# Performance work log

Measured on AMD Instinct MI355X. Metric: run time of the kernel, lower is better.

Reference implementation:

```python
import jax, jax.numpy as jnp
import numpy as np

VOCAB, E, H, P, B, S = 30522, 1024, 1024, 16, 32, 256
HD = H // 2  # per-direction LSTM hidden


def _lstm_dir(xt, Wih, Whh, bih, bhh, reverse):
    # xt: [S,B,in]; PyTorch gate order i,f,g,o
    Hd = Whh.shape[1]
    Bz = xt.shape[1]
    bias = bih + bhh

    def step(carry, xb):
        h, c = carry
        g = xb @ Wih.T + h @ Whh.T + bias
        i, f, gg, o = jnp.split(g, 4, axis=-1)
        c = jax.nn.sigmoid(f) * c + jax.nn.sigmoid(i) * jnp.tanh(gg)
        h = jax.nn.sigmoid(o) * jnp.tanh(c)
        return (h, c), h

    init = (jnp.zeros((Bz, Hd), xt.dtype), jnp.zeros((Bz, Hd), xt.dtype))
    _, hs = jax.lax.scan(step, init, xt, reverse=reverse)
    return hs  # [S,B,Hd], time-ordered


def _bilstm(x, Wih, Whh, bih, bhh):
    # x: [B,S,in]; Wih: [2,4*HD,in] (dir 0 = fwd, dir 1 = bwd)
    xt = jnp.swapaxes(x, 0, 1)
    fw = _lstm_dir(xt, Wih[0], Whh[0], bih[0], bhh[0], False)
    bw = _lstm_dir(xt, Wih[1], Whh[1], bih[1], bhh[1], True)
    return jnp.swapaxes(jnp.concatenate([fw, bw], axis=-1), 0, 1)  # [B,S,2*HD]


def setup_inputs() -> dict:
    key = jax.random.key(0)
    ks = jax.random.split(key, 20)
    sc = 0.05
    inp = {}
    inp["emb"] = jax.random.normal(ks[0], (VOCAB, E), jnp.float32) * sc
    inp["ctx_emb"] = jax.random.normal(ks[1], (VOCAB, E), jnp.float32) * sc
    inp["prompt_emb"] = jax.random.normal(ks[2], (P, E), jnp.float32) * sc
    # LSTM layer 0: input E; layer 1: input 2*HD = H
    inp["Wih0"] = jax.random.normal(ks[3], (2, 4 * HD, E), jnp.float32) * sc
    inp["Whh0"] = jax.random.normal(ks[4], (2, 4 * HD, HD), jnp.float32) * sc
    inp["bih0"] = jax.random.normal(ks[5], (2, 4 * HD), jnp.float32) * sc
    inp["bhh0"] = jax.random.normal(ks[6], (2, 4 * HD), jnp.float32) * sc
    inp["Wih1"] = jax.random.normal(ks[7], (2, 4 * HD, H), jnp.float32) * sc
    inp["Whh1"] = jax.random.normal(ks[8], (2, 4 * HD, HD), jnp.float32) * sc
    inp["bih1"] = jax.random.normal(ks[9], (2, 4 * HD), jnp.float32) * sc
    inp["bhh1"] = jax.random.normal(ks[10], (2, 4 * HD), jnp.float32) * sc
    inp["W1"] = jax.random.normal(ks[11], (H, H), jnp.float32) * sc
    inp["b1"] = jnp.zeros((H,), jnp.float32)
    inp["W2"] = jax.random.normal(ks[12], (E, H), jnp.float32) * sc
    inp["b2"] = jnp.zeros((E,), jnp.float32)
    inp["input_ids"] = jax.random.randint(ks[13], (B, S), 0, VOCAB)
    # distinct, sorted prompt positions per batch row (torch loop assumes valid slots)
    pk = jax.random.split(ks[14], B)
    perms = jax.vmap(lambda k: jax.random.permutation(k, S)[:P])(pk)
    inp["prompt_indexes"] = jnp.sort(perms, axis=1)
    return inp


def reference(emb, ctx_emb, prompt_emb, Wih0, Whh0, bih0, bhh0,
              Wih1, Whh1, bih1, bhh1, W1, b1, W2, b2,
              input_ids, prompt_indexes):
    raw = emb[input_ids]                               # [B,S,E]
    b_idx = jnp.arange(input_ids.shape[0])[:, None]    # [B,1]
    # unique_prompt branch: detached raw + ctx embedding, scatter prompt embeds
    allb = jax.lax.stop_gradient(raw) + ctx_emb[input_ids]
    allb = allb.at[b_idx, prompt_indexes].set(
        jnp.broadcast_to(prompt_emb, (input_ids.shape[0],) + prompt_emb.shape))
    h = _bilstm(allb, Wih0, Whh0, bih0, bhh0)
    h = _bilstm(h, Wih1, Whh1, bih1, bhh1)             # [B,S,H]
    out = jax.nn.relu(h @ W1.T + b1) @ W2.T + b2       # [B,S,E]
    upd = out[b_idx, prompt_indexes] + prompt_emb      # [B,P,E]
    return raw.at[b_idx, prompt_indexes].set(upd)
```

## Files before the change

kernel.cpp:

```cpp
#include <hip/hip_runtime.h>
#include <hip/hip_bf16.h>
#include <math.h>

constexpr int NB  = 32;
constexpr int NS  = 256;
constexpr int NE  = 1024;
constexpr int NH  = 1024;
constexpr int NHD = 512;
constexpr int NG  = 2048;
constexpr int NP  = 16;
constexpr int NBS = NB * NS;
constexpr int GK  = 1024;

constexpr int UPW  = 16;
constexpr int NWGD = NHD / UPW;
constexpr size_t GT_DIR = (size_t)NWGD * 256 * 2048;

typedef __attribute__((ext_vector_type(8))) short bf16x8;
typedef __attribute__((ext_vector_type(4))) float f32x4;
typedef unsigned short u16;

__device__ __forceinline__ float sigm(float x) { return 1.0f / (1.0f + __expf(-x)); }
__device__ __forceinline__ u16 f2bf(float f) {
    union { float f; unsigned u; } v; v.f = f;
    unsigned r = v.u + 0x7FFF + ((v.u >> 16) & 1);
    return (u16)(r >> 16);
}
__device__ __forceinline__ float bf2f(u16 b) {
    return __uint_as_float((unsigned)b << 16);
}

__global__ void k_zero(int* p) { p[blockIdx.x * 256 + threadIdx.x] = 0; }

__global__ void k_allb(const float* __restrict__ emb, const float* __restrict__ ctx,
                       const float* __restrict__ pemb, const int* __restrict__ ids,
                       const int* __restrict__ pidx, u16* __restrict__ allb) {
    int r = blockIdx.x;
    int b = r >> 8, s = r & 255;
    __shared__ int ppos;
    if (threadIdx.x == 0) {
        int t = -1;
        #pragma unroll
        for (int p = 0; p < NP; ++p)
            if (pidx[b * NP + p] == s) t = p;
        ppos = t;
    }
    __syncthreads();
    int e = threadIdx.x;
    float4 v;
    if (ppos >= 0) {
        v = ((const float4*)(pemb + (size_t)ppos * NE))[e];
    } else {
        int id = ids[r];
        float4 a = ((const float4*)(emb + (size_t)id * NE))[e];
        float4 c = ((const float4*)(ctx + (size_t)id * NE))[e];
        v = make_float4(a.x + c.x, a.y + c.y, a.z + c.z, a.w + c.w);
    }
    ushort4 o;
    o.x = f2bf(v.x); o.y = f2bf(v.y); o.z = f2bf(v.z); o.w = f2bf(v.w);
    *(ushort4*)(allb + ((size_t)(s * NB + b)) * NE + e * 4) = o;
}

__global__ void k_raw(const float* __restrict__ emb, const int* __restrict__ ids,
                      float* __restrict__ out) {
    int r = blockIdx.x;
    int id = ids[r];
    ((float4*)(out + (size_t)r * NE))[threadIdx.x] =
        ((const float4*)(emb + (size_t)id * NE))[threadIdx.x];
}

__global__ void k_wcvt(const float* __restrict__ Wih, const float* __restrict__ bih,
                       const float* __restrict__ bhh, u16* __restrict__ Wbf,
                       float* __restrict__ biasC) {
    int blk = blockIdx.x;
    int d = blk >> 11, np = blk & 2047;
    int rw = (np & 3) * 512 + (np >> 2);
    const float* src = Wih + ((size_t)d * NG + rw) * GK;
    u16* dst = Wbf + ((size_t)d * NG + np) * GK;
    int t = threadIdx.x;
    float4 v = ((const float4*)src)[t];
    ushort4 o;
    o.x = f2bf(v.x); o.y = f2bf(v.y); o.z = f2bf(v.z); o.w = f2bf(v.w);
    ((ushort4*)dst)[t] = o;
    if (t == 0)
        biasC[d * NG + np] = bih[d * NG + rw] + bhh[d * NG + rw];
}

__global__ __launch_bounds__(256) void k_gemm_m(const u16* __restrict__ A0,
                                                const u16* __restrict__ A1,
                                                int astride,
                                                const u16* __restrict__ W,
                                                const float* __restrict__ bc,
                                                float* __restrict__ Gt) {
    __shared__ char At[128 * 128];
    __shared__ char Wt[128 * 128];
    int tid = threadIdx.x;
    int lane = tid & 63, w = tid >> 6;
    int n0 = blockIdx.x * 128, m0 = blockIdx.y * 128;
    int r = tid >> 1, h = tid & 1;

    f32x4 acc[4][4];
    #pragma unroll
    for (int i = 0; i < 4; ++i)
        #pragma unroll
        for (int j = 0; j < 4; ++j) acc[i][j] = (f32x4){0.f, 0.f, 0.f, 0.f};

    unsigned rsw = (unsigned)((r & 7) << 4);
    for (int kt = 0; kt < GK; kt += 64) {
        {
            int k0 = kt + h * 32;
            const u16* asrc = (k0 < 512) ? (A0 + (size_t)(m0 + r) * astride + k0)
                                         : (A1 + (size_t)(m0 + r) * astride + (k0 - 512));
            const u16* wsrc = W + (size_t)(n0 + r) * GK + k0;
            #pragma unroll
            for (int j = 0; j < 4; ++j) {
                uint4 va = *(const uint4*)(asrc + j * 8);
                *(uint4*)(At + r * 128 + (((unsigned)(h * 64 + j * 16)) ^ rsw)) = va;
                uint4 vw = *(const uint4*)(wsrc + j * 8);
                *(uint4*)(Wt + r * 128 + (((unsigned)(h * 64 + j * 16)) ^ rsw)) = vw;
            }
        }
        __syncthreads();
        #pragma unroll
        for (int sub = 0; sub < 2; ++sub) {
            bf16x8 af[4], bfr[4];
            int kbyte = sub * 64 + (lane >> 4) * 16;
            #pragma unroll
            for (int ni = 0; ni < 4; ++ni) {
                int rr = (w & 1) * 64 + ni * 16 + (lane & 15);
                af[ni] = *(const bf16x8*)(Wt + rr * 128 + ((unsigned)kbyte ^ ((unsigned)((rr & 7) << 4))));
            }
            #pragma unroll
            for (int mi = 0; mi < 4; ++mi) {
                int rr = (w >> 1) * 64 + mi * 16 + (lane & 15);
                bfr[mi] = *(const bf16x8*)(At + rr * 128 + ((unsigned)kbyte ^ ((unsigned)((rr & 7) << 4))));
            }
            #pragma unroll
            for (int mi = 0; mi < 4; ++mi)
                #pragma unroll
                for (int ni = 0; ni < 4; ++ni)
                    acc[mi][ni] = __builtin_amdgcn_mfma_f32_16x16x32_bf16(
                        af[ni], bfr[mi], acc[mi][ni], 0, 0, 0);
        }
        __syncthreads();
    }
    #pragma unroll
    for (int mi = 0; mi < 4; ++mi) {
        int mp = m0 + (w >> 1) * 64 + mi * 16 + (lane & 15);
        int t = mp >> 5, b = mp & 31;
        #pragma unroll
        for (int ni = 0; ni < 4; ++ni) {
            int npb = n0 + (w & 1) * 64 + ni * 16 + (lane >> 4) * 4;
            int unit = npb >> 2;
            float4 bv = *(const float4*)(bc + npb);
            f32x4 a = acc[mi][ni];
            float4 o = make_float4(a[0] + bv.x, a[1] + bv.y, a[2] + bv.z, a[3] + bv.w);
            *(float4*)(Gt + ((size_t)((unit >> 4) * NS + t)) * 2048 + b * 64 + (unit & 15) * 4) = o;
        }
    }
}

__global__ __launch_bounds__(256) void k_lstm_p(const float* __restrict__ Gt,
                                                const float* __restrict__ Whh,
                                                u16* __restrict__ hxb,
                                                int* __restrict__ cblk) {
    __shared__ char hlds[NB * NHD * 2];
    int wg = blockIdx.x;
    int d = wg & 1;
    int slice = wg >> 1;
    int n0 = slice * UPW;
    int tid = threadIdx.x;
    int lane = tid & 63;
    int w = tid >> 6;
    int* lines  = cblk + d * 512;
    int* myline = lines + slice * 16;
    int pollidx = (lane & 31) * 16;
    u16* hxd = hxb + (size_t)d * NS * NB * NHD;
    const float* Gd = Gt + (size_t)d * GT_DIR + (size_t)slice * NS * 2048;

    bf16x8 wfrag[16];
    {
        int rloc = lane & 15;
        int usub = rloc >> 2, g = rloc & 3;
        int kb = lane >> 4;
        const float* wrow = Whh + ((size_t)d * NG + g * NHD + n0 + 4 * w + usub) * NHD;
        #pragma unroll
        for (int kk = 0; kk < 16; ++kk) {
            const float* p = wrow + kk * 32 + kb * 8;
            float4 x = *(const float4*)p;
            float4 y = *(const float4*)(p + 4);
            bf16x8 wf;
            wf[0] = (short)f2bf(x.x); wf[1] = (short)f2bf(x.y);
            wf[2] = (short)f2bf(x.z); wf[3] = (short)f2bf(x.w);
            wf[4] = (short)f2bf(y.x); wf[5] = (short)f2bf(y.y);
            wf[6] = (short)f2bf(y.z); wf[7] = (short)f2bf(y.w);
            wfrag[kk] = wf;
        }
    }
    int uloc  = 4 * w + (lane >> 4);
    int unitC = n0 + uloc;
    int bcol0 = lane & 15;
    int bcol1 = 16 + bcol0;
    int kb    = lane >> 4;
    int c8 = tid & 7, bRow = tid >> 3;

    float c0 = 0.f, c1 = 0.f;
    int ttp = d ? (NS - 1) : 0;
    float4 Gv0 = *(const float4*)(Gd + (size_t)ttp * 2048 + bcol0 * 64 + uloc * 4);
    float4 Gv1 = *(const float4*)(Gd + (size_t)ttp * 2048 + bcol1 * 64 + uloc * 4);

    for (int step = 0; step < NS; ++step) {
        int tt = d ? (NS - 1 - step) : step;
        f32x4 acc0 = {0.f, 0.f, 0.f, 0.f};
        f32x4 acc1 = {0.f, 0.f, 0.f, 0.f};
        if (step) {
            int tprev = d ? tt + 1 : tt - 1;
            const u16* srow = hxd + ((size_t)tprev * NB + bRow) * NHD;
            char* dstrow = hlds + bRow * 1024;
            unsigned rsw = (unsigned)((bRow & 7) << 4);
            #pragma unroll
            for (int i = 0; i < 8; ++i) {
                uint4 v = *(const uint4*)(srow + c8 * 64 + i * 8);
                *(uint4*)(dstrow + (((unsigned)(c8 * 128 + i * 16)) ^ rsw)) = v;
            }
            __syncthreads();
            const char* b0base = hlds + bcol0 * 1024;
            const char* b1base = hlds + bcol1 * 1024;
            unsigned s0 = (unsigned)((bcol0 & 7) << 4);
            unsigned s1 = (unsigned)((bcol1 & 7) << 4);
            #pragma unroll
            for (int kk = 0; kk < 16; ++kk) {
                bf16x8 b0 = *(const bf16x8*)(b0base + (((unsigned)(kk * 64 + kb * 16)) ^ s0));
                bf16x8 b1 = *(const bf16x8*)(b1base + (((unsigned)(kk * 64 + kb * 16)) ^ s1));
                acc0 = __builtin_amdgcn_mfma_f32_16x16x32_bf16(wfrag[kk], b0, acc0, 0, 0, 0);
                acc1 = __builtin_amdgcn_mfma_f32_16x16x32_bf16(wfrag[kk], b1, acc1, 0, 0, 0);
            }
        }
        {
            float ig = sigm(acc0[0] + Gv0.x);
            float fg = sigm(acc0[1] + Gv0.y);
            float gg = tanhf(acc0[2] + Gv0.z);
            float og = sigm(acc0[3] + Gv0.w);
            c0 = fg * c0 + ig * gg;
            float hv = og * tanhf(c0);
            __hip_atomic_store(hxd + ((size_t)tt * NB + bcol0) * NHD + unitC, f2bf(hv),
                               __ATOMIC_RELAXED, __HIP_MEMORY_SCOPE_AGENT);
        }
        {
            float ig = sigm(acc1[0] + Gv1.x);
            float fg = sigm(acc1[1] + Gv1.y);
            float gg = tanhf(acc1[2] + Gv1.z);
            float og = sigm(acc1[3] + Gv1.w);
            c1 = fg * c1 + ig * gg;
            float hv = og * tanhf(c1);
            __hip_atomic_store(hxd + ((size_t)tt * NB + bcol1) * NHD + unitC, f2bf(hv),
                               __ATOMIC_RELAXED, __HIP_MEMORY_SCOPE_AGENT);
        }
        if (step == NS - 1) break;
        asm volatile("s_waitcnt vmcnt(0)" ::: "memory");
        __syncthreads();
        if (tid == 0)
            __hip_atomic_store(myline, step + 1, __ATOMIC_RELAXED,
                               __HIP_MEMORY_SCOPE_AGENT);
        {
            int ttn = d ? tt - 1 : tt + 1;
            Gv0 = *(const float4*)(Gd + (size_t)ttn * 2048 + bcol0 * 64 + uloc * 4);
            Gv1 = *(const float4*)(Gd + (size_t)ttn * 2048 + bcol1 * 64 + uloc * 4);
        }
        asm volatile("" ::: "memory");
        {
            int target = step + 1;
            for (;;) {
                int v = __hip_atomic_load(lines + pollidx, __ATOMIC_RELAXED,
                                          __HIP_MEMORY_SCOPE_AGENT);
                if (__all(v >= target)) break;
                __builtin_amdgcn_s_sleep(1);
            }
        }
    }
}

__global__ __launch_bounds__(256) void k_mlp1(const u16* __restrict__ hxb,
                                              const int* __restrict__ pidx,
                                              const float* __restrict__ W1,
                                              const float* __restrict__ b1,
                                              float* __restrict__ mid) {
    __shared__ float As[16][65];
    __shared__ float Ws[16][65];
    int tid = threadIdx.x;
    int tx = tid & 15, ty = tid >> 4;
    int n0 = blockIdx.x * 64, m0 = blockIdx.y * 64;
    int lr = tid >> 2;
    int lk = (tid & 3) * 4;
    int m = m0 + lr;
    int bb = m >> 4;
    int s = pidx[m];
    float acc[4][4] = {};
    for (int kt = 0; kt < GK; kt += 16) {
        int k0 = kt + lk;
        int half = k0 >> 9;
        ushort4 av4 = *(const ushort4*)(hxb + (((size_t)(half * NS + s)) * NB + bb) * NHD + (k0 & 511));
        float4 wv = *(const float4*)(W1 + (size_t)(n0 + lr) * GK + k0);
        As[lk + 0][lr] = bf2f(av4.x); As[lk + 1][lr] = bf2f(av4.y);
        As[lk + 2][lr] = bf2f(av4.z); As[lk + 3][lr] = bf2f(av4.w);
        Ws[lk + 0][lr] = wv.x; Ws[lk + 1][lr] = wv.y;
        Ws[lk + 2][lr] = wv.z; Ws[lk + 3][lr] = wv.w;
        __syncthreads();
        #pragma unroll
        for (int kk = 0; kk < 16; ++kk) {
            float a[4], wv2[4];
            #pragma unroll
            for (int i = 0; i < 4; ++i) a[i] = As[kk][ty * 4 + i];
            #pragma unroll
            for (int j = 0; j < 4; ++j) wv2[j] = Ws[kk][tx * 4 + j];
            #pragma unroll
            for (int i = 0; i < 4; ++i)
                #pragma unroll
                for (int j = 0; j < 4; ++j) acc[i][j] += a[i] * wv2[j];
        }
        __syncthreads();
    }
    #pragma unroll
    for (int j = 0; j < 4; ++j) {
        int n = n0 + tx * 4 + j;
        float bias = b1[n];
        #pragma unroll
        for (int i = 0; i < 4; ++i)
            mid[(size_t)(m0 + ty * 4 + i) * 1024 + n] = fmaxf(acc[i][j] + bias, 0.f);
    }
}

__global__ __launch_bounds__(256) void k_mlp2(const float* __restrict__ mid,
                                              const int* __restrict__ pidx,
                                              const float* __restrict__ W2,
                                              const float* __restrict__ b2,
                                              const float* __restrict__ pemb,
                                              float* __restrict__ out) {
    __shared__ float As[16][65];
    __shared__ float Ws[16][65];
    int tid = threadIdx.x;
    int tx = tid & 15, ty = tid >> 4;
    int n0 = blockIdx.x * 64, m0 = blockIdx.y * 64;
    int lr = tid >> 2;
    int lk = (tid & 3) * 4;
    float acc[4][4] = {};
    for (int kt = 0; kt < GK; kt += 16) {
        float4 av = *(const float4*)(mid + (size_t)(m0 + lr) * GK + kt + lk);
        float4 wv = *(const float4*)(W2 + (size_t)(n0 + lr) * GK + kt + lk);
        As[lk + 0][lr] = av.x; As[lk + 1][lr] = av.y;
        As[lk + 2][lr] = av.z; As[lk + 3][lr] = av.w;
        Ws[lk + 0][lr] = wv.x; Ws[lk + 1][lr] = wv.y;
        Ws[lk + 2][lr] = wv.z; Ws[lk + 3][lr] = wv.w;
        __syncthreads();
        #pragma unroll
        for (int kk = 0; kk < 16; ++kk) {
            float a[4], wv2[4];
            #pragma unroll
            for (int i = 0; i < 4; ++i) a[i] = As[kk][ty * 4 + i];
            #pragma unroll
            for (int j = 0; j < 4; ++j) wv2[j] = Ws[kk][tx * 4 + j];
            #pragma unroll
            for (int i = 0; i < 4; ++i)
                #pragma unroll
                for (int j = 0; j < 4; ++j) acc[i][j] += a[i] * wv2[j];
        }
        __syncthreads();
    }
    #pragma unroll
    for (int i = 0; i < 4; ++i) {
        int m = m0 + ty * 4 + i;
        int bb = m >> 4, p = m & 15;
        int s = pidx[m];
        float* orow = out + ((size_t)(bb * NS + s)) * NE;
        const float* prow = pemb + (size_t)p * NE;
        #pragma unroll
        for (int j = 0; j < 4; ++j) {
            int n = n0 + tx * 4 + j;
            orow[n] = acc[i][j] + b2[n] + prow[n];
        }
    }
}

extern "C" void kernel_launch(void* const* d_in, const int* in_sizes, int n_in,
                              void* d_out, int out_size, void* d_ws, size_t ws_size,
                              hipStream_t stream) {
    const float* emb  = (const float*)d_in[0];
    const float* ctx  = (const float*)d_in[1];
    const float* pemb = (const float*)d_in[2];
    const float* Wih0 = (const float*)d_in[3];
    const float* Whh0 = (const float*)d_in[4];
    const float* bih0 = (const float*)d_in[5];
    const float* bhh0 = (const float*)d_in[6];
    const float* Wih1 = (const float*)d_in[7];
    const float* Whh1 = (const float*)d_in[8];
    const float* bih1 = (const float*)d_in[9];
    const float* bhh1 = (const float*)d_in[10];
    const float* W1   = (const float*)d_in[11];
    const float* b1   = (const float*)d_in[12];
    const float* W2   = (const float*)d_in[13];
    const float* b2   = (const float*)d_in[14];
    const int* ids    = (const int*)d_in[15];
    const int* pidx   = (const int*)d_in[16];
    float* out = (float*)d_out;

    char* ws = (char*)d_ws;
    float* Gt    = (float*)ws;
    u16*   allb  = (u16*)(ws + 134217728u);
    u16*   hx    = (u16*)(ws + 150994944u);
    u16*   Wbf   = (u16*)(ws + 167772160u);
    float* biasC = (float*)(ws + 176160768u);
    float* mid   = (float*)(ws + 176177152u);
    int*   ctr   = (int*)(ws + 178274304u);

    k_zero<<<dim3(8), dim3(256), 0, stream>>>(ctr);
    k_allb<<<dim3(NBS), dim3(256), 0, stream>>>(emb, ctx, pemb, ids, pidx, allb);

    k_wcvt<<<dim3(2 * NG), dim3(256), 0, stream>>>(Wih0, bih0, bhh0, Wbf, biasC);
    for (int d = 0; d < 2; ++d)
        k_gemm_m<<<dim3(NG / 128, NBS / 128), dim3(256), 0, stream>>>(
            allb, allb + 512, 1024, Wbf + (size_t)d * NG * GK, biasC + d * NG,
            Gt + (size_t)d * GT_DIR);
    k_lstm_p<<<dim3(2 * NWGD), dim3(256), 0, stream>>>(Gt, Whh0, hx, ctr);

    k_raw<<<dim3(NBS), dim3(256), 0, stream>>>(emb, ids, out);

    k_wcvt<<<dim3(2 * NG), dim3(256), 0, stream>>>(Wih1, bih1, bhh1, Wbf, biasC);
    for (int d = 0; d < 2; ++d)
        k_gemm_m<<<dim3(NG / 128, NBS / 128), dim3(256), 0, stream>>>(
            hx, hx + (size_t)NS * NB * NHD, 512, Wbf + (size_t)d * NG * GK,
            biasC + d * NG, Gt + (size_t)d * GT_DIR);
    k_lstm_p<<<dim3(2 * NWGD), dim3(256), 0, stream>>>(Gt, Whh1, hx, ctr + 1024);

    k_mlp1<<<dim3(16, 8), dim3(256), 0, stream>>>(hx, pidx, W1, b1, mid);
    k_mlp2<<<dim3(16, 8), dim3(256), 0, stream>>>(mid, pidx, W2, b2, pemb, out);
}
```

Measured before the change: 2.363 ms.

## Split LSTM batch into two halves with separate flags to overlap sync and compute

The persistent LSTM recurrence kernel now treats the 32 batch columns as two independent 16-column halves, each with its own LDS buffer and its own cross-workgroup completion counters. While one half waits on the grid-wide flag and loads its hidden state, the other half runs its MFMA and gate computation, so barrier latency is hidden behind useful work. The gate activations also switch to fast exp/divide based sigmoid and tanh approximations. The cost is twice as many barriers and flag stores per step, double the counter memory, and a slight loss of accuracy in the activations.

```diff
diff --git a/kernel.cpp b/kernel.cpp
--- a/kernel.cpp
+++ b/kernel.cpp
@@ -20,7 +20,13 @@
 typedef __attribute__((ext_vector_type(4))) float f32x4;
 typedef unsigned short u16;
 
-__device__ __forceinline__ float sigm(float x) { return 1.0f / (1.0f + __expf(-x)); }
+__device__ __forceinline__ float sigm(float x) {
+    return __fdividef(1.0f, 1.0f + __expf(-x));
+}
+__device__ __forceinline__ float tanhfast(float x) {
+    float t = __expf(2.0f * x);
+    return 1.0f - __fdividef(2.0f, t + 1.0f);
+}
 __device__ __forceinline__ u16 f2bf(float f) {
     union { float f; unsigned u; } v; v.f = f;
     unsigned r = v.u + 0x7FFF + ((v.u >> 16) & 1);
@@ -160,11 +166,12 @@
     }
 }
 
-__global__ __launch_bounds__(256) void k_lstm_p(const float* __restrict__ Gt,
+__global__ __launch_bounds__(256) void k_lstm_q(const float* __restrict__ Gt,
                                                 const float* __restrict__ Whh,
                                                 u16* __restrict__ hxb,
                                                 int* __restrict__ cblk) {
-    __shared__ char hlds[NB * NHD * 2];
+    __shared__ char hldsA[16 * 1024];
+    __shared__ char hldsB[16 * 1024];
     int wg = blockIdx.x;
     int d = wg & 1;
     int slice = wg >> 1;
@@ -172,9 +179,11 @@
     int tid = threadIdx.x;
     int lane = tid & 63;
     int w = tid >> 6;
-    int* lines  = cblk + d * 512;
-    int* myline = lines + slice * 16;
-    int pollidx = (lane & 31) * 16;
+    int* linesA  = cblk + d * 1024;
+    int* linesB  = linesA + 512;
+    int* mylineA = linesA + slice * 16;
+    int* mylineB = linesB + slice * 16;
+    int pollidx  = (lane & 31) * 16;
     u16* hxd = hxb + (size_t)d * NS * NB * NHD;
     const float* Gd = Gt + (size_t)d * GT_DIR + (size_t)slice * NS * 2048;
 
@@ -182,11 +191,11 @@
     {
         int rloc = lane & 15;
         int usub = rloc >> 2, g = rloc & 3;
-        int kb = lane >> 4;
+        int kb0 = lane >> 4;
         const float* wrow = Whh + ((size_t)d * NG + g * NHD + n0 + 4 * w + usub) * NHD;
         #pragma unroll
         for (int kk = 0; kk < 16; ++kk) {
-            const float* p = wrow + kk * 32 + kb * 8;
+            const float* p = wrow + kk * 32 + kb0 * 8;
             float4 x = *(const float4*)p;
             float4 y = *(const float4*)(p + 4);
             bf16x8 wf;
@@ -199,84 +208,113 @@
     }
     int uloc  = 4 * w + (lane >> 4);
     int unitC = n0 + uloc;
-    int bcol0 = lane & 15;
-    int bcol1 = 16 + bcol0;
+    int bA    = lane & 15;
+    int bB    = 16 + bA;
     int kb    = lane >> 4;
-    int c8 = tid & 7, bRow = tid >> 3;
-
-    float c0 = 0.f, c1 = 0.f;
-    int ttp = d ? (NS - 1) : 0;
-    float4 Gv0 = *(const float4*)(Gd + (size_t)ttp * 2048 + bcol0 * 64 + uloc * 4);
-    float4 Gv1 = *(const float4*)(Gd + (size_t)ttp * 2048 + bcol1 * 64 + uloc * 4);
+    unsigned rdsw = (unsigned)((bA & 7) << 4);
+    int sRow = tid >> 4;
+    int sC   = tid & 15;
+    unsigned srsw = (unsigned)((sRow & 7) << 4);
+
+    float cA = 0.f, cB = 0.f;
+    uint4 stA[4], stB[4];
+    int tt0 = d ? (NS - 1) : 0;
+    float4 GvA = *(const float4*)(Gd + (size_t)tt0 * 2048 + bA * 64 + uloc * 4);
+    float4 GvB = *(const float4*)(Gd + (size_t)tt0 * 2048 + bB * 64 + uloc * 4);
 
     for (int step = 0; step < NS; ++step) {
         int tt = d ? (NS - 1 - step) : step;
-        f32x4 acc0 = {0.f, 0.f, 0.f, 0.f};
-        f32x4 acc1 = {0.f, 0.f, 0.f, 0.f};
+        f32x4 accA = {0.f, 0.f, 0.f, 0.f};
         if (step) {
-            int tprev = d ? tt + 1 : tt - 1;
-            const u16* srow = hxd + ((size_t)tprev * NB + bRow) * NHD;
-            char* dstrow = hlds + bRow * 1024;
-            unsigned rsw = (unsigned)((bRow & 7) << 4);
-            #pragma unroll
-            for (int i = 0; i < 8; ++i) {
-                uint4 v = *(const uint4*)(srow + c8 * 64 + i * 8);
-                *(uint4*)(dstrow + (((unsigned)(c8 * 128 + i * 16)) ^ rsw)) = v;
+            const char* abase = hldsA + bA * 1024;
+            #pragma unroll
+            for (int kk = 0; kk < 16; ++kk) {
+                bf16x8 bfv = *(const bf16x8*)(abase + (((unsigned)(kk * 64 + kb * 16)) ^ rdsw));
+                accA = __builtin_amdgcn_mfma_f32_16x16x32_bf16(wfrag[kk], bfv, accA, 0, 0, 0);
             }
-            __syncthreads();
-            const char* b0base = hlds + bcol0 * 1024;
-            const char* b1base = hlds + bcol1 * 1024;
-            unsigned s0 = (unsigned)((bcol0 & 7) << 4);
-            unsigned s1 = (unsigned)((bcol1 & 7) << 4);
+        }
+        {
+            float ig = sigm(accA[0] + GvA.x);
+            float fg = sigm(accA[1] + GvA.y);
+            float gg = tanhfast(accA[2] + GvA.z);
+            float og = sigm(accA[3] + GvA.w);
+            cA = fg * cA + ig * gg;
+            float hv = og * tanhfast(cA);
+            __hip_atomic_store(hxd + ((size_t)tt * NB + bA) * NHD + unitC, f2bf(hv),
+                               __ATOMIC_RELAXED, __HIP_MEMORY_SCOPE_AGENT);
+        }
+        if (step) {
+            char* dr = hldsB + sRow * 1024;
+            #pragma unroll
+            for (int i = 0; i < 4; ++i)
+                *(uint4*)(dr + (((unsigned)(sC * 64 + i * 16)) ^ srsw)) = stB[i];
+        }
+        asm volatile("s_waitcnt vmcnt(0)" ::: "memory");
+        __syncthreads();
+        if (tid == 0)
+            __hip_atomic_store(mylineA, step + 1, __ATOMIC_RELAXED,
+                               __HIP_MEMORY_SCOPE_AGENT);
+        f32x4 accB = {0.f, 0.f, 0.f, 0.f};
+        if (step) {
+            const char* bbase = hldsB + bA * 1024;
             #pragma unroll
             for (int kk = 0; kk < 16; ++kk) {
-                bf16x8 b0 = *(const bf16x8*)(b0base + (((unsigned)(kk * 64 + kb * 16)) ^ s0));
-                bf16x8 b1 = *(const bf16x8*)(b1base + (((unsigned)(kk * 64 + kb * 16)) ^ s1));
-                acc0 = __builtin_amdgcn_mfma_f32_16x16x32_bf16(wfrag[kk], b0, acc0, 0, 0, 0);
-                acc1 = __builtin_amdgcn_mfma_f32_16x16x32_bf16(wfrag[kk], b1, acc1, 0, 0, 0);
+                bf16x8 bfv = *(const bf16x8*)(bbase + (((unsigned)(kk * 64 + kb * 16)) ^ rdsw));
+                accB = __builtin_amdgcn_mfma_f32_16x16x32_bf16(wfrag[kk], bfv, accB, 0, 0, 0);
             }
         }
         {
-            float ig = sigm(acc0[0] + Gv0.x);
-            float fg = sigm(acc0[1] + Gv0.y);
-            float gg = tanhf(acc0[2] + Gv0.z);
-            float og = sigm(acc0[3] + Gv0.w);
-            c0 = fg * c0 + ig * gg;
-            float hv = og * tanhf(c0);
-            __hip_atomic_store(hxd + ((size_t)tt * NB + bcol0) * NHD + unitC, f2bf(hv),
+            float ig = sigm(accB[0] + GvB.x);
+            float fg = sigm(accB[1] + GvB.y);
+            float gg = tanhfast(accB[2] + GvB.z);
+            float og = sigm(accB[3] + GvB.w);
+            cB = fg * cB + ig * gg;
+            float hv = og * tanhfast(cB);
+            __hip_atomic_store(hxd + ((size_t)tt * NB + bB) * NHD + unitC, f2bf(hv),
                                __ATOMIC_RELAXED, __HIP_MEMORY_SCOPE_AGENT);
         }
-        {
-            float ig = sigm(acc1[0] + Gv1.x);
-            float fg = sigm(acc1[1] + Gv1.y);
-            float gg = tanhf(acc1[2] + Gv1.z);
-            float og = sigm(acc1[3] + Gv1.w);
-            c1 = fg * c1 + ig * gg;
-            float hv = og * tanhf(c1);
-            __hip_atomic_store(hxd + ((size_t)tt * NB + bcol1) * NHD + unitC, f2bf(hv),
-                               __ATOMIC_RELAXED, __HIP_MEMORY_SCOPE_AGENT);
-        }
+        asm volatile("s_waitcnt vmcnt(0)" ::: "memory");
+        __syncthreads();
+        if (tid == 0)
+            __hip_atomic_store(mylineB, step + 1, __ATOMIC_RELAXED,
+                               __HIP_MEMORY_SCOPE_AGENT);
         if (step == NS - 1) break;
-        asm volatile("s_waitcnt vmcnt(0)" ::: "memory");
-        __syncthreads();
-        if (tid == 0)
-            __hip_atomic_store(myline, step + 1, __ATOMIC_RELAXED,
-                               __HIP_MEMORY_SCOPE_AGENT);
+        int target = step + 1;
+        for (;;) {
+            int v = __hip_atomic_load(linesA + pollidx, __ATOMIC_RELAXED,
+                                      __HIP_MEMORY_SCOPE_AGENT);
+            if (__all(v >= target)) break;
+            __builtin_amdgcn_s_sleep(1);
+        }
         {
             int ttn = d ? tt - 1 : tt + 1;
-            Gv0 = *(const float4*)(Gd + (size_t)ttn * 2048 + bcol0 * 64 + uloc * 4);
-            Gv1 = *(const float4*)(Gd + (size_t)ttn * 2048 + bcol1 * 64 + uloc * 4);
+            GvA = *(const float4*)(Gd + (size_t)ttn * 2048 + bA * 64 + uloc * 4);
+            GvB = *(const float4*)(Gd + (size_t)ttn * 2048 + bB * 64 + uloc * 4);
+        }
+        {
+            const u16* sa = hxd + ((size_t)tt * NB + sRow) * NHD + sC * 32;
+            #pragma unroll
+            for (int i = 0; i < 4; ++i) stA[i] = *(const uint4*)(sa + i * 8);
         }
         asm volatile("" ::: "memory");
-        {
-            int target = step + 1;
-            for (;;) {
-                int v = __hip_atomic_load(lines + pollidx, __ATOMIC_RELAXED,
-                                          __HIP_MEMORY_SCOPE_AGENT);
-                if (__all(v >= target)) break;
-                __builtin_amdgcn_s_sleep(1);
-            }
-        }
+        for (;;) {
+            int v = __hip_atomic_load(linesB + pollidx, __ATOMIC_RELAXED,
+                                      __HIP_MEMORY_SCOPE_AGENT);
+            if (__all(v >= target)) break;
+            __builtin_amdgcn_s_sleep(1);
+        }
+        {
+            char* da = hldsA + sRow * 1024;
+            #pragma unroll
+            for (int i = 0; i < 4; ++i)
+                *(uint4*)(da + (((unsigned)(sC * 64 + i * 16)) ^ srsw)) = stA[i];
+        }
+        {
+            const u16* sb = hxd + ((size_t)tt * NB + 16 + sRow) * NHD + sC * 32;
+            #pragma unroll
+            for (int i = 0; i < 4; ++i) stB[i] = *(const uint4*)(sb + i * 8);
+        }
+        __syncthreads();
     }
 }
 
@@ -412,7 +450,7 @@
     float* mid   = (float*)(ws + 176177152u);
     int*   ctr   = (int*)(ws + 178274304u);
 
-    k_zero<<<dim3(8), dim3(256), 0, stream>>>(ctr);
+    k_zero<<<dim3(16), dim3(256), 0, stream>>>(ctr);
     k_allb<<<dim3(NBS), dim3(256), 0, stream>>>(emb, ctx, pemb, ids, pidx, allb);
 
     k_wcvt<<<dim3(2 * NG), dim3(256), 0, stream>>>(Wih0, bih0, bhh0, Wbf, biasC);
@@ -420,7 +458,7 @@
         k_gemm_m<<<dim3(NG / 128, NBS / 128), dim3(256), 0, stream>>>(
             allb, allb + 512, 1024, Wbf + (size_t)d * NG * GK, biasC + d * NG,
             Gt + (size_t)d * GT_DIR);
-    k_lstm_p<<<dim3(2 * NWGD), dim3(256), 0, stream>>>(Gt, Whh0, hx, ctr);
+    k_lstm_q<<<dim3(2 * NWGD), dim3(256), 0, stream>>>(Gt, Whh0, hx, ctr);
 
     k_raw<<<dim3(NBS), dim3(256), 0, stream>>>(emb, ids, out);
 
@@ -429,7 +467,7 @@
         k_gemm_m<<<dim3(NG / 128, NBS / 128), dim3(256), 0, stream>>>(
             hx, hx + (size_t)NS * NB * NHD, 512, Wbf + (size_t)d * NG * GK,
             biasC + d * NG, Gt + (size_t)d * GT_DIR);
-    k_lstm_p<<<dim3(2 * NWGD), dim3(256), 0, stream>>>(Gt, Whh1, hx, ctr + 1024);
+    k_lstm_q<<<dim3(2 * NWGD), dim3(256), 0, stream>>>(Gt, Whh1, hx, ctr + 2048);
 
     k_mlp1<<<dim3(16, 8), dim3(256), 0, stream>>>(hx, pidx, W1, b1, mid);
     k_mlp2<<<dim3(16, 8), dim3(256), 0, stream>>>(mid, pidx, W2, b2, pemb, out);
```

New measurement: 2.797 ms. +18.4%, slower.

## Replace LSTM step counters with sentinel-filled hidden state polling

Applied to the files above, without the earlier changes.

The persistent recurrent LSTM kernel no longer signals each step through per-workgroup counter lines. It pre-fills the hidden-state buffer with a NaN sentinel pattern, and consumers poll the actual h data until no sentinel remains. This removes the store-drain wait and barrier before the flag write, and merges the data fetch with the synchronization. Each step's h stores are also staged through LDS into 64-bit stores, and tanh/sigmoid use fast exp-based forms. The cost is two extra fill kernels over the hx buffer, plus reliance on no real h value bit-matching the sentinel.

```diff
diff --git a/kernel.cpp b/kernel.cpp
--- a/kernel.cpp
+++ b/kernel.cpp
@@ -19,8 +19,15 @@
 typedef __attribute__((ext_vector_type(8))) short bf16x8;
 typedef __attribute__((ext_vector_type(4))) float f32x4;
 typedef unsigned short u16;
-
-__device__ __forceinline__ float sigm(float x) { return 1.0f / (1.0f + __expf(-x)); }
+typedef unsigned long long u64;
+
+__device__ __forceinline__ float sigm(float x) {
+    return __fdividef(1.0f, 1.0f + __expf(-x));
+}
+__device__ __forceinline__ float tanhfast(float x) {
+    float t = __expf(2.0f * x);
+    return 1.0f - __fdividef(2.0f, t + 1.0f);
+}
 __device__ __forceinline__ u16 f2bf(float f) {
     union { float f; unsigned u; } v; v.f = f;
     unsigned r = v.u + 0x7FFF + ((v.u >> 16) & 1);
@@ -29,8 +36,16 @@
 __device__ __forceinline__ float bf2f(u16 b) {
     return __uint_as_float((unsigned)b << 16);
 }
-
-__global__ void k_zero(int* p) { p[blockIdx.x * 256 + threadIdx.x] = 0; }
+constexpr u16 SENT = 0x7FC1;
+__device__ __forceinline__ bool hasSent(u64 v) {
+    u64 x = v ^ 0x7FC17FC17FC17FC1ULL;
+    return ((x - 0x0001000100010001ULL) & ~x & 0x8000800080008000ULL) != 0ULL;
+}
+
+__global__ void k_fill(uint4* p) {
+    p[blockIdx.x * 256 + threadIdx.x] =
+        make_uint4(0x7FC17FC1u, 0x7FC17FC1u, 0x7FC17FC1u, 0x7FC17FC1u);
+}
 
 __global__ void k_allb(const float* __restrict__ emb, const float* __restrict__ ctx,
                        const float* __restrict__ pemb, const int* __restrict__ ids,
@@ -160,11 +175,11 @@
     }
 }
 
-__global__ __launch_bounds__(256) void k_lstm_p(const float* __restrict__ Gt,
+__global__ __launch_bounds__(256) void k_lstm_r(const float* __restrict__ Gt,
                                                 const float* __restrict__ Whh,
-                                                u16* __restrict__ hxb,
-                                                int* __restrict__ cblk) {
+                                                u16* __restrict__ hxb) {
     __shared__ char hlds[NB * NHD * 2];
+    __shared__ u16 hstg[NB][UPW];
     int wg = blockIdx.x;
     int d = wg & 1;
     int slice = wg >> 1;
@@ -172,9 +187,6 @@
     int tid = threadIdx.x;
     int lane = tid & 63;
     int w = tid >> 6;
-    int* lines  = cblk + d * 512;
-    int* myline = lines + slice * 16;
-    int pollidx = (lane & 31) * 16;
     u16* hxd = hxb + (size_t)d * NS * NB * NHD;
     const float* Gd = Gt + (size_t)d * GT_DIR + (size_t)slice * NS * 2048;
 
@@ -182,11 +194,11 @@
     {
         int rloc = lane & 15;
         int usub = rloc >> 2, g = rloc & 3;
-        int kb = lane >> 4;
+        int kb0 = lane >> 4;
         const float* wrow = Whh + ((size_t)d * NG + g * NHD + n0 + 4 * w + usub) * NHD;
         #pragma unroll
         for (int kk = 0; kk < 16; ++kk) {
-            const float* p = wrow + kk * 32 + kb * 8;
+            const float* p = wrow + kk * 32 + kb0 * 8;
             float4 x = *(const float4*)p;
             float4 y = *(const float4*)(p + 4);
             bf16x8 wf;
@@ -199,12 +211,15 @@
     }
     int uloc  = 4 * w + (lane >> 4);
     int unitC = n0 + uloc;
+    (void)unitC;
     int bcol0 = lane & 15;
     int bcol1 = 16 + bcol0;
     int kb    = lane >> 4;
     int c8 = tid & 7, bRow = tid >> 3;
+    unsigned rsw = (unsigned)((bRow & 7) << 4);
 
     float c0 = 0.f, c1 = 0.f;
+    u64 st[16];
     int ttp = d ? (NS - 1) : 0;
     float4 Gv0 = *(const float4*)(Gd + (size_t)ttp * 2048 + bcol0 * 64 + uloc * 4);
     float4 Gv1 = *(const float4*)(Gd + (size_t)ttp * 2048 + bcol1 * 64 + uloc * 4);
@@ -214,13 +229,11 @@
         f32x4 acc0 = {0.f, 0.f, 0.f, 0.f};
         f32x4 acc1 = {0.f, 0.f, 0.f, 0.f};
         if (step) {
-            int tprev = d ? tt + 1 : tt - 1;
-            const u16* srow = hxd + ((size_t)tprev * NB + bRow) * NHD;
             char* dstrow = hlds + bRow * 1024;
-            unsigned rsw = (unsigned)((bRow & 7) << 4);
             #pragma unroll
             for (int i = 0; i < 8; ++i) {
-                uint4 v = *(const uint4*)(srow + c8 * 64 + i * 8);
+                uint4 v = make_uint4((unsigned)st[2 * i], (unsigned)(st[2 * i] >> 32),
+                                     (unsigned)st[2 * i + 1], (unsigned)(st[2 * i + 1] >> 32));
                 *(uint4*)(dstrow + (((unsigned)(c8 * 128 + i * 16)) ^ rsw)) = v;
             }
             __syncthreads();
@@ -239,42 +252,51 @@
         {
             float ig = sigm(acc0[0] + Gv0.x);
             float fg = sigm(acc0[1] + Gv0.y);
-            float gg = tanhf(acc0[2] + Gv0.z);
+            float gg = tanhfast(acc0[2] + Gv0.z);
             float og = sigm(acc0[3] + Gv0.w);
             c0 = fg * c0 + ig * gg;
-            float hv = og * tanhf(c0);
-            __hip_atomic_store(hxd + ((size_t)tt * NB + bcol0) * NHD + unitC, f2bf(hv),
-                               __ATOMIC_RELAXED, __HIP_MEMORY_SCOPE_AGENT);
+            hstg[bcol0][uloc] = f2bf(og * tanhfast(c0));
         }
         {
             float ig = sigm(acc1[0] + Gv1.x);
             float fg = sigm(acc1[1] + Gv1.y);
-            float gg = tanhf(acc1[2] + Gv1.z);
+            float gg = tanhfast(acc1[2] + Gv1.z);
             float og = sigm(acc1[3] + Gv1.w);
             c1 = fg * c1 + ig * gg;
-            float hv = og * tanhf(c1);
-            __hip_atomic_store(hxd + ((size_t)tt * NB + bcol1) * NHD + unitC, f2bf(hv),
-                               __ATOMIC_RELAXED, __HIP_MEMORY_SCOPE_AGENT);
-        }
+            hstg[bcol1][uloc] = f2bf(og * tanhfast(c1));
+        }
+        __syncthreads();
+        if (tid < 128) {
+            int bcolS = tid & 31, q = tid >> 5;
+            u64 v = *(const u64*)&hstg[bcolS][q * 4];
+            __hip_atomic_store((u64*)(hxd + ((size_t)tt * NB + bcolS) * NHD + n0 + q * 4),
+                               v, __ATOMIC_RELAXED, __HIP_MEMORY_SCOPE_AGENT);
+        }
+        asm volatile("" ::: "memory");
         if (step == NS - 1) break;
-        asm volatile("s_waitcnt vmcnt(0)" ::: "memory");
-        __syncthreads();
-        if (tid == 0)
-            __hip_atomic_store(myline, step + 1, __ATOMIC_RELAXED,
-                               __HIP_MEMORY_SCOPE_AGENT);
         {
             int ttn = d ? tt - 1 : tt + 1;
             Gv0 = *(const float4*)(Gd + (size_t)ttn * 2048 + bcol0 * 64 + uloc * 4);
             Gv1 = *(const float4*)(Gd + (size_t)ttn * 2048 + bcol1 * 64 + uloc * 4);
         }
-        asm volatile("" ::: "memory");
         {
-            int target = step + 1;
+            const u64* src = (const u64*)(hxd + ((size_t)tt * NB + bRow) * NHD + c8 * 64);
+            #pragma unroll
+            for (int j = 0; j < 16; ++j)
+                st[j] = __hip_atomic_load(src + j, __ATOMIC_RELAXED,
+                                          __HIP_MEMORY_SCOPE_AGENT);
             for (;;) {
-                int v = __hip_atomic_load(lines + pollidx, __ATOMIC_RELAXED,
-                                          __HIP_MEMORY_SCOPE_AGENT);
-                if (__all(v >= target)) break;
+                unsigned pend = 0;
+                #pragma unroll
+                for (int j = 0; j < 16; ++j)
+                    pend |= (hasSent(st[j]) ? 1u : 0u) << j;
+                if (!pend) break;
                 __builtin_amdgcn_s_sleep(1);
+                #pragma unroll
+                for (int j = 0; j < 16; ++j)
+                    if (pend & (1u << j))
+                        st[j] = __hip_atomic_load(src + j, __ATOMIC_RELAXED,
+                                                  __HIP_MEMORY_SCOPE_AGENT);
             }
         }
     }
@@ -410,9 +432,8 @@
     u16*   Wbf   = (u16*)(ws + 167772160u);
     float* biasC = (float*)(ws + 176160768u);
     float* mid   = (float*)(ws + 176177152u);
-    int*   ctr   = (int*)(ws + 178274304u);
-
-    k_zero<<<dim3(8), dim3(256), 0, stream>>>(ctr);
+
+    k_fill<<<dim3(4096), dim3(256), 0, stream>>>((uint4*)hx);
     k_allb<<<dim3(NBS), dim3(256), 0, stream>>>(emb, ctx, pemb, ids, pidx, allb);
 
     k_wcvt<<<dim3(2 * NG), dim3(256), 0, stream>>>(Wih0, bih0, bhh0, Wbf, biasC);
@@ -420,7 +441,7 @@
         k_gemm_m<<<dim3(NG / 128, NBS / 128), dim3(256), 0, stream>>>(
             allb, allb + 512, 1024, Wbf + (size_t)d * NG * GK, biasC + d * NG,
             Gt + (size_t)d * GT_DIR);
-    k_lstm_p<<<dim3(2 * NWGD), dim3(256), 0, stream>>>(Gt, Whh0, hx, ctr);
+    k_lstm_r<<<dim3(2 * NWGD), dim3(256), 0, stream>>>(Gt, Whh0, hx);
 
     k_raw<<<dim3(NBS), dim3(256), 0, stream>>>(emb, ids, out);
 
@@ -429,7 +450,8 @@
         k_gemm_m<<<dim3(NG / 128, NBS / 128), dim3(256), 0, stream>>>(
             hx, hx + (size_t)NS * NB * NHD, 512, Wbf + (size_t)d * NG * GK,
             biasC + d * NG, Gt + (size_t)d * GT_DIR);
-    k_lstm_p<<<dim3(2 * NWGD), dim3(256), 0, stream>>>(Gt, Whh1, hx, ctr + 1024);
+    k_fill<<<dim3(4096), dim3(256), 0, stream>>>((uint4*)hx);
+    k_lstm_r<<<dim3(2 * NWGD), dim3(256), 0, stream>>>(Gt, Whh1, hx);
 
     k_mlp1<<<dim3(16, 8), dim3(256), 0, stream>>>(hx, pidx, W1, b1, mid);
     k_mlp2<<<dim3(16, 8), dim3(256), 0, stream>>>(mid, pidx, W2, b2, pemb, out);
```

Measured after the change: 3.262 ms. 38.0% more time.

## Use per-wave completion flags, prefetch hidden state, pack stores, fast tanh

Applied to the files above, without the earlier changes.

The persistent LSTM recurrence kernel now has each wave publish its own completion flag, so the block-wide barrier before signalling is gone. After polling all 128 wave flags, each thread loads the next step's hidden state into registers. The LDS tile is double-buffered so the next step's writes can't clobber data still being read. Hidden outputs are gathered with shuffles into 64-bit packed stores instead of scattered 16-bit atomics, and tanh/sigmoid use fast exp/divide approximations; this adds polling traffic and some approximation error.

```diff
diff --git a/kernel.cpp b/kernel.cpp
--- a/kernel.cpp
+++ b/kernel.cpp
@@ -19,8 +19,15 @@
 typedef __attribute__((ext_vector_type(8))) short bf16x8;
 typedef __attribute__((ext_vector_type(4))) float f32x4;
 typedef unsigned short u16;
-
-__device__ __forceinline__ float sigm(float x) { return 1.0f / (1.0f + __expf(-x)); }
+typedef unsigned long long u64;
+
+__device__ __forceinline__ float sigm(float x) {
+    return __fdividef(1.0f, 1.0f + __expf(-x));
+}
+__device__ __forceinline__ float tanhfast(float x) {
+    float t = __expf(2.0f * x);
+    return 1.0f - __fdividef(2.0f, t + 1.0f);
+}
 __device__ __forceinline__ u16 f2bf(float f) {
     union { float f; unsigned u; } v; v.f = f;
     unsigned r = v.u + 0x7FFF + ((v.u >> 16) & 1);
@@ -160,11 +167,11 @@
     }
 }
 
-__global__ __launch_bounds__(256) void k_lstm_p(const float* __restrict__ Gt,
+__global__ __launch_bounds__(256) void k_lstm_w(const float* __restrict__ Gt,
                                                 const float* __restrict__ Whh,
                                                 u16* __restrict__ hxb,
                                                 int* __restrict__ cblk) {
-    __shared__ char hlds[NB * NHD * 2];
+    __shared__ char hlds[2][NB * NHD * 2];
     int wg = blockIdx.x;
     int d = wg & 1;
     int slice = wg >> 1;
@@ -172,9 +179,10 @@
     int tid = threadIdx.x;
     int lane = tid & 63;
     int w = tid >> 6;
-    int* lines  = cblk + d * 512;
-    int* myline = lines + slice * 16;
-    int pollidx = (lane & 31) * 16;
+    int* lines  = cblk + d * 2048;
+    int* myline = lines + (slice * 4 + w) * 16;
+    int pidx0 = lane * 16;
+    int pidx1 = (lane + 64) * 16;
     u16* hxd = hxb + (size_t)d * NS * NB * NHD;
     const float* Gd = Gt + (size_t)d * GT_DIR + (size_t)slice * NS * 2048;
 
@@ -182,11 +190,11 @@
     {
         int rloc = lane & 15;
         int usub = rloc >> 2, g = rloc & 3;
-        int kb = lane >> 4;
+        int kb0 = lane >> 4;
         const float* wrow = Whh + ((size_t)d * NG + g * NHD + n0 + 4 * w + usub) * NHD;
         #pragma unroll
         for (int kk = 0; kk < 16; ++kk) {
-            const float* p = wrow + kk * 32 + kb * 8;
+            const float* p = wrow + kk * 32 + kb0 * 8;
             float4 x = *(const float4*)p;
             float4 y = *(const float4*)(p + 4);
             bf16x8 wf;
@@ -199,12 +207,18 @@
     }
     int uloc  = 4 * w + (lane >> 4);
     int unitC = n0 + uloc;
+    (void)unitC;
     int bcol0 = lane & 15;
     int bcol1 = 16 + bcol0;
     int kb    = lane >> 4;
-    int c8 = tid & 7, bRow = tid >> 3;
+    int sRow = 8 * w + (lane >> 3);
+    int c8   = lane & 7;
+    unsigned rsw = (unsigned)((sRow & 7) << 4);
+    unsigned s0 = (unsigned)((bcol0 & 7) << 4);
+    unsigned s1 = (unsigned)((bcol1 & 7) << 4);
 
     float c0 = 0.f, c1 = 0.f;
+    uint4 st[8];
     int ttp = d ? (NS - 1) : 0;
     float4 Gv0 = *(const float4*)(Gd + (size_t)ttp * 2048 + bcol0 * 64 + uloc * 4);
     float4 Gv1 = *(const float4*)(Gd + (size_t)ttp * 2048 + bcol1 * 64 + uloc * 4);
@@ -214,20 +228,14 @@
         f32x4 acc0 = {0.f, 0.f, 0.f, 0.f};
         f32x4 acc1 = {0.f, 0.f, 0.f, 0.f};
         if (step) {
-            int tprev = d ? tt + 1 : tt - 1;
-            const u16* srow = hxd + ((size_t)tprev * NB + bRow) * NHD;
-            char* dstrow = hlds + bRow * 1024;
-            unsigned rsw = (unsigned)((bRow & 7) << 4);
-            #pragma unroll
-            for (int i = 0; i < 8; ++i) {
-                uint4 v = *(const uint4*)(srow + c8 * 64 + i * 8);
-                *(uint4*)(dstrow + (((unsigned)(c8 * 128 + i * 16)) ^ rsw)) = v;
-            }
+            char* tile = hlds[step & 1];
+            char* dstrow = tile + sRow * 1024;
+            #pragma unroll
+            for (int i = 0; i < 8; ++i)
+                *(uint4*)(dstrow + (((unsigned)(c8 * 128 + i * 16)) ^ rsw)) = st[i];
             __syncthreads();
-            const char* b0base = hlds + bcol0 * 1024;
-            const char* b1base = hlds + bcol1 * 1024;
-            unsigned s0 = (unsigned)((bcol0 & 7) << 4);
-            unsigned s1 = (unsigned)((bcol1 & 7) << 4);
+            const char* b0base = tile + bcol0 * 1024;
+            const char* b1base = tile + bcol1 * 1024;
             #pragma unroll
             for (int kk = 0; kk < 16; ++kk) {
                 bf16x8 b0 = *(const bf16x8*)(b0base + (((unsigned)(kk * 64 + kb * 16)) ^ s0));
@@ -236,30 +244,44 @@
                 acc1 = __builtin_amdgcn_mfma_f32_16x16x32_bf16(wfrag[kk], b1, acc1, 0, 0, 0);
             }
         }
+        unsigned v0, v1;
         {
             float ig = sigm(acc0[0] + Gv0.x);
             float fg = sigm(acc0[1] + Gv0.y);
-            float gg = tanhf(acc0[2] + Gv0.z);
+            float gg = tanhfast(acc0[2] + Gv0.z);
             float og = sigm(acc0[3] + Gv0.w);
             c0 = fg * c0 + ig * gg;
-            float hv = og * tanhf(c0);
-            __hip_atomic_store(hxd + ((size_t)tt * NB + bcol0) * NHD + unitC, f2bf(hv),
-                               __ATOMIC_RELAXED, __HIP_MEMORY_SCOPE_AGENT);
+            v0 = (unsigned)f2bf(og * tanhfast(c0));
         }
         {
             float ig = sigm(acc1[0] + Gv1.x);
             float fg = sigm(acc1[1] + Gv1.y);
-            float gg = tanhf(acc1[2] + Gv1.z);
+            float gg = tanhfast(acc1[2] + Gv1.z);
             float og = sigm(acc1[3] + Gv1.w);
             c1 = fg * c1 + ig * gg;
-            float hv = og * tanhf(c1);
-            __hip_atomic_store(hxd + ((size_t)tt * NB + bcol1) * NHD + unitC, f2bf(hv),
-                               __ATOMIC_RELAXED, __HIP_MEMORY_SCOPE_AGENT);
+            v1 = (unsigned)f2bf(og * tanhfast(c1));
+        }
+        {
+            int bl = lane & 15;
+            unsigned a0 = __shfl(v0, bl);
+            unsigned a1 = __shfl(v0, bl + 16);
+            unsigned a2 = __shfl(v0, bl + 32);
+            unsigned a3 = __shfl(v0, bl + 48);
+            unsigned b0 = __shfl(v1, bl);
+            unsigned b1 = __shfl(v1, bl + 16);
+            unsigned b2 = __shfl(v1, bl + 32);
+            unsigned b3 = __shfl(v1, bl + 48);
+            bool lo = (lane < 16);
+            unsigned k0 = lo ? a0 : b0, k1 = lo ? a1 : b1;
+            unsigned k2 = lo ? a2 : b2, k3 = lo ? a3 : b3;
+            u64 val = (u64)(k0 | (k1 << 16)) | ((u64)(k2 | (k3 << 16)) << 32);
+            if (lane < 32)
+                __hip_atomic_store((u64*)(hxd + ((size_t)tt * NB + lane) * NHD + n0 + 4 * w),
+                                   val, __ATOMIC_RELAXED, __HIP_MEMORY_SCOPE_AGENT);
         }
         if (step == NS - 1) break;
         asm volatile("s_waitcnt vmcnt(0)" ::: "memory");
-        __syncthreads();
-        if (tid == 0)
+        if (lane == 0)
             __hip_atomic_store(myline, step + 1, __ATOMIC_RELAXED,
                                __HIP_MEMORY_SCOPE_AGENT);
         {
@@ -271,11 +293,19 @@
         {
             int target = step + 1;
             for (;;) {
-                int v = __hip_atomic_load(lines + pollidx, __ATOMIC_RELAXED,
+                int a = __hip_atomic_load(lines + pidx0, __ATOMIC_RELAXED,
                                           __HIP_MEMORY_SCOPE_AGENT);
-                if (__all(v >= target)) break;
+                int b = __hip_atomic_load(lines + pidx1, __ATOMIC_RELAXED,
+                                          __HIP_MEMORY_SCOPE_AGENT);
+                if (__all(a >= target && b >= target)) break;
                 __builtin_amdgcn_s_sleep(1);
             }
+        }
+        asm volatile("" ::: "memory");
+        {
+            const u16* srow = hxd + ((size_t)tt * NB + sRow) * NHD + c8 * 64;
+            #pragma unroll
+            for (int i = 0; i < 8; ++i) st[i] = *(const uint4*)(srow + i * 8);
         }
     }
 }
@@ -412,7 +442,7 @@
     float* mid   = (float*)(ws + 176177152u);
     int*   ctr   = (int*)(ws + 178274304u);
 
-    k_zero<<<dim3(8), dim3(256), 0, stream>>>(ctr);
+    k_zero<<<dim3(32), dim3(256), 0, stream>>>(ctr);
     k_allb<<<dim3(NBS), dim3(256), 0, stream>>>(emb, ctx, pemb, ids, pidx, allb);
 
     k_wcvt<<<dim3(2 * NG), dim3(256), 0, stream>>>(Wih0, bih0, bhh0, Wbf, biasC);
@@ -420,7 +450,7 @@
         k_gemm_m<<<dim3(NG / 128, NBS / 128), dim3(256), 0, stream>>>(
             allb, allb + 512, 1024, Wbf + (size_t)d * NG * GK, biasC + d * NG,
             Gt + (size_t)d * GT_DIR);
-    k_lstm_p<<<dim3(2 * NWGD), dim3(256), 0, stream>>>(Gt, Whh0, hx, ctr);
+    k_lstm_w<<<dim3(2 * NWGD), dim3(256), 0, stream>>>(Gt, Whh0, hx, ctr);
 
     k_raw<<<dim3(NBS), dim3(256), 0, stream>>>(emb, ids, out);
 
@@ -429,7 +459,7 @@
         k_gemm_m<<<dim3(NG / 128, NBS / 128), dim3(256), 0, stream>>>(
             hx, hx + (size_t)NS * NB * NHD, 512, Wbf + (size_t)d * NG * GK,
             biasC + d * NG, Gt + (size_t)d * GT_DIR);
-    k_lstm_p<<<dim3(2 * NWGD), dim3(256), 0, stream>>>(Gt, Whh1, hx, ctr + 1024);
+    k_lstm_w<<<dim3(2 * NWGD), dim3(256), 0, stream>>>(Gt, Whh1, hx, ctr + 4096);
 
     k_mlp1<<<dim3(16, 8), dim3(256), 0, stream>>>(hx, pidx, W1, b1, mid);
     k_mlp2<<<dim3(16, 8), dim3(256), 0, stream>>>(mid, pidx, W2, b2, pemb, out);
```

After: 3.626 ms. +53.4%, slower.
